# Kernel tuning notes

Hardware: AMD Instinct MI355X
Metric: run time of the kernel (lower is better)

Reference implementation:

```python
import jax, jax.numpy as jnp
import numpy as np

N = 100000
E = 1600000
IN_C, HID_C, OUT_C = 64, 64, 32


def setup_inputs() -> dict:
    key = jax.random.key(0)
    ks = jax.random.split(key, 8)
    x = jax.random.normal(ks[0], (N, IN_C), dtype=jnp.float32)
    edge_index = jax.random.randint(ks[1], (2, E), 0, N, dtype=jnp.int64)
    # GCNConv weights (glorot-ish scale) and biases
    W1 = jax.random.normal(ks[2], (IN_C, HID_C), dtype=jnp.float32) / np.sqrt(IN_C)
    b1 = jnp.zeros((HID_C,), dtype=jnp.float32)
    W2 = jax.random.normal(ks[3], (HID_C, HID_C), dtype=jnp.float32) / np.sqrt(HID_C)
    b2 = jnp.zeros((HID_C,), dtype=jnp.float32)
    Wlin = jax.random.normal(ks[4], (HID_C, OUT_C), dtype=jnp.float32) / np.sqrt(HID_C)
    blin = jnp.zeros((OUT_C,), dtype=jnp.float32)
    return {"x": x, "edge_index": edge_index, "W1": W1, "b1": b1,
            "W2": W2, "b2": b2, "Wlin": Wlin, "blin": blin}


def _gcn_norm(edge_index):
    # PyG GCNConv default: add self-loops, symmetric normalization.
    loop = jnp.arange(N, dtype=edge_index.dtype)
    row = jnp.concatenate([edge_index[0], loop])  # source nodes [E+N]
    col = jnp.concatenate([edge_index[1], loop])  # target nodes [E+N]
    deg = jax.ops.segment_sum(jnp.ones_like(col, dtype=jnp.float32), col,
                              num_segments=N)
    dinv = jnp.where(deg > 0, deg ** -0.5, 0.0)
    norm = dinv[row] * dinv[col]  # [E+N]
    return row, col, norm


def _gcn_conv(h, W, b, row, col, norm):
    h = h @ W                                  # [N, F_out]
    msg = h[row] * norm[:, None]               # gather + scale, [E+N, F_out]
    out = jax.ops.segment_sum(msg, col, num_segments=N)  # scatter-add
    return out + b


def reference(x, edge_index, W1, b1, W2, b2, Wlin, blin):
    row, col, norm = _gcn_norm(edge_index)
    h = jax.nn.relu(_gcn_conv(x, W1, b1, row, col, norm))
    h = jax.nn.relu(_gcn_conv(h, W2, b2, row, col, norm))
    return h @ Wlin + blin
```

## Files before the change

### kernel.cpp

```cpp
#include <hip/hip_runtime.h>
#include <hip/hip_fp16.h>

#define IN_C 64
#define HID_C 64
#define OUT_C 32
#define S_NODES  512
#define S_CAP  12288
#define CHUNK_E 2048

typedef _Float16 f16_t;
typedef f16_t f16x2 __attribute__((ext_vector_type(2)));

__device__ __forceinline__ float dot2(unsigned int a, unsigned int b, float c) {
#if __has_builtin(__builtin_amdgcn_fdot2)
    return __builtin_amdgcn_fdot2(*(f16x2*)&a, *(f16x2*)&b, c, false);
#else
    float2 af = __half22float2(*(__half2*)&a);
    float2 bf = __half22float2(*(__half2*)&b);
    return fmaf(af.x, bf.x, fmaf(af.y, bf.y, c));
#endif
}

__global__ void prep(const int* ei32, int* flag, int n_check,
                     const float* __restrict__ W1, const float* __restrict__ W2,
                     const float* __restrict__ Wlin,
                     unsigned short* __restrict__ Wh1,
                     unsigned short* __restrict__ Wh2,
                     unsigned short* __restrict__ Whl) {
    __shared__ int s_any;
    if (threadIdx.x == 0) s_any = 0;
    __syncthreads();
    int any = 0;
    for (int i = threadIdx.x; i < n_check; i += blockDim.x) {
        if (ei32[2 * i + 1] != 0) any = 1;
    }
    if (any) atomicOr(&s_any, 1);
    for (int i = threadIdx.x; i < 4096; i += 256) {
        int r = i >> 6, c = i & 63;
        f16_t h1 = (f16_t)W1[r * 64 + c];
        f16_t h2 = (f16_t)W2[r * 64 + c];
        Wh1[c * 64 + r] = *(unsigned short*)&h1;
        Wh2[c * 64 + r] = *(unsigned short*)&h2;
    }
    for (int i = threadIdx.x; i < 2048; i += 256) {
        int r = i >> 5, c = i & 31;
        f16_t h = (f16_t)Wlin[r * 32 + c];
        Whl[c * 64 + r] = *(unsigned short*)&h;
    }
    __syncthreads();
    if (threadIdx.x == 0) *flag = (s_any == 0) ? 1 : 0;
}

__device__ __forceinline__ int ld_edge(const void* ei, int idx, int is64) {
    if (is64) return (int)((const long long*)ei)[idx];
    return ((const int*)ei)[idx];
}

__global__ __launch_bounds__(256) void bin_edges(const void* ei, int E, const int* flag,
                                                 int* bcur, int NB,
                                                 int* __restrict__ staging) {
    __shared__ int cnt[256], boff[256], lcur[256], gbase[256];
    __shared__ int stg[CHUNK_E];
    __shared__ int s_is64;
    int tid = threadIdx.x;
    if (tid == 0) s_is64 = *flag;
    cnt[tid] = 0;
    __syncthreads();
    int is64 = s_is64;
    int e0 = blockIdx.x * CHUNK_E;
    int e1 = min(E, e0 + CHUNK_E);
    for (int e = e0 + tid; e < e1; e += 256) {
        int dst = ld_edge(ei, E + e, is64);
        atomicAdd(&cnt[dst >> 9], 1);
    }
    __syncthreads();
    int v = cnt[tid];
    gbase[tid] = v;
    __syncthreads();
    for (int o = 1; o < 256; o <<= 1) {
        int u = (tid >= o) ? gbase[tid - o] : 0;
        __syncthreads();
        gbase[tid] += u;
        __syncthreads();
    }
    boff[tid] = gbase[tid] - v;
    lcur[tid] = boff[tid];
    __syncthreads();
    for (int e = e0 + tid; e < e1; e += 256) {
        int src = ld_edge(ei, e, is64);
        int dst = ld_edge(ei, E + e, is64);
        int p = atomicAdd(&lcur[dst >> 9], 1);
        stg[p] = src | ((dst & 511) << 17);
    }
    __syncthreads();
    if (tid < NB && cnt[tid] > 0) gbase[tid] = atomicAdd(&bcur[tid], cnt[tid]);
    __syncthreads();
    int sw = tid >> 4, sl = tid & 15;
    for (int b = sw; b < NB; b += 16) {
        int c = cnt[b];
        if (c == 0) continue;
        int o = boff[b], g = gbase[b];
        size_t gb = (size_t)b * S_CAP;
        for (int j = sl; j < c; j += 16) {
            if (g + j < S_CAP) staging[gb + g + j] = stg[o + j];
        }
    }
}

__global__ __launch_bounds__(256) void place_fine(const int* __restrict__ staging,
                                                  const int* __restrict__ bcur,
                                                  int* __restrict__ offs,
                                                  float* __restrict__ dinv,
                                                  int* __restrict__ rec, int N, int NB) {
    __shared__ int sdeg[S_NODES];
    __shared__ int tsum[256];
    __shared__ int curs[S_NODES];
    __shared__ int sb[256];
    int tid = threadIdx.x;
    int vcnt = (tid < NB) ? min(bcur[tid], S_CAP) : 0;
    sb[tid] = vcnt;
    sdeg[tid] = 0;
    sdeg[tid + 256] = 0;
    __syncthreads();
    for (int o = 1; o < 256; o <<= 1) {
        int u = (tid >= o) ? sb[tid - o] : 0;
        __syncthreads();
        sb[tid] += u;
        __syncthreads();
    }
    int cnt = min(bcur[blockIdx.x], S_CAP);
    int bbase = sb[blockIdx.x] - cnt;
    if (blockIdx.x == NB - 1 && tid == 0) offs[N] = sb[255];
    int base = blockIdx.x * S_NODES;
    int nn = min(S_NODES, N - base);
    size_t sbase = (size_t)blockIdx.x * S_CAP;
    for (int j = tid; j < cnt; j += 256) atomicAdd(&sdeg[staging[sbase + j] >> 17], 1);
    __syncthreads();
    int d0 = sdeg[2 * tid], d1 = sdeg[2 * tid + 1];
    tsum[tid] = d0 + d1;
    __syncthreads();
    for (int o = 1; o < 256; o <<= 1) {
        int v = (tid >= o) ? tsum[tid - o] : 0;
        __syncthreads();
        tsum[tid] += v;
        __syncthreads();
    }
    int pre = bbase + ((tid == 0) ? 0 : tsum[tid - 1]);
    curs[2 * tid] = pre;
    curs[2 * tid + 1] = pre + d0;
    if (2 * tid < nn) {
        offs[base + 2 * tid] = pre;
        dinv[base + 2 * tid] = rsqrtf((float)(d0 + 1));
    }
    if (2 * tid + 1 < nn) {
        offs[base + 2 * tid + 1] = pre + d0;
        dinv[base + 2 * tid + 1] = rsqrtf((float)(d1 + 1));
    }
    __syncthreads();
    for (int j = tid; j < cnt; j += 256) {
        int pk = staging[sbase + j];
        int p = atomicAdd(&curs[pk >> 17], 1);
        rec[p] = pk & 0x1FFFF;
    }
}

template <int IN_F32>
__global__ __launch_bounds__(256) void gemm64(const void* __restrict__ in,
                                              const unsigned short* __restrict__ Wh,
                                              unsigned short* __restrict__ out,
                                              const float* __restrict__ dinv, int n) {
    __shared__ uint4 sA[32 * 8];
    int tid = threadIdx.x;
    int lane = tid & 63, wave = tid >> 6;
    unsigned int wu[32];
    {
        const uint4* col = (const uint4*)(Wh + (size_t)lane * 64);
#pragma unroll
        for (int j = 0; j < 8; j++) {
            uint4 w4 = col[j];
            wu[4 * j] = w4.x; wu[4 * j + 1] = w4.y;
            wu[4 * j + 2] = w4.z; wu[4 * j + 3] = w4.w;
        }
    }
    int base = blockIdx.x * 32;
    if (IN_F32) {
        const float2* A2 = (const float2*)in;
        int lim = n * 32;
        for (int i = tid; i < 1024; i += 256) {
            int gi = base * 32 + i;
            float2 v = (gi < lim) ? A2[gi] : make_float2(0.f, 0.f);
            ((__half2*)sA)[i] = __floats2half2_rn(v.x, v.y);
        }
    } else {
        const uint2* A2 = (const uint2*)in;
        int lim = n * 16;
        for (int i = tid; i < 512; i += 256) {
            int gi = base * 16 + i;
            ((uint2*)sA)[i] = (gi < lim) ? A2[gi] : make_uint2(0u, 0u);
        }
    }
    __syncthreads();
    int r0 = base + wave * 8;
    int r1 = min(r0 + 8, n);
    for (int r = r0; r < r1; r++) {
        int rr = r - base;
        float a0 = 0.f, a1 = 0.f;
#pragma unroll
        for (int j = 0; j < 8; j++) {
            uint4 u = sA[rr * 8 + j];
            a0 = dot2(u.x, wu[4 * j], a0);
            a1 = dot2(u.y, wu[4 * j + 1], a1);
            a0 = dot2(u.z, wu[4 * j + 2], a0);
            a1 = dot2(u.w, wu[4 * j + 3], a1);
        }
        __half hv = __float2half_rn((a0 + a1) * dinv[r]);
        out[(size_t)r * 64 + lane] = *(unsigned short*)&hv;
    }
}

__global__ void aggregate(const unsigned short* __restrict__ t,
                          const int* __restrict__ offs, const int* __restrict__ rec,
                          const float* __restrict__ dinv, const float* __restrict__ bias,
                          unsigned short* __restrict__ acc, int n) {
    int wave = (blockIdx.x * blockDim.x + threadIdx.x) >> 6;
    int lane = threadIdx.x & 63;
    if (wave >= n) return;
    int g = lane >> 3;
    int gl = lane & 7;
    int beg = offs[wave], end = offs[wave + 1];
    int m = end - beg + 1;
    const uint4* t4 = (const uint4*)t;
    float s[8] = {0.f, 0.f, 0.f, 0.f, 0.f, 0.f, 0.f, 0.f};
    for (int i = 0; i < m; i += 32) {
        int srcs[4];
        float ws[4];
#pragma unroll
        for (int u = 0; u < 4; u++) {
            int it = i + u * 8 + g;
            srcs[u] = (it == 0) ? wave : ((it < m) ? rec[beg + it - 1] : wave);
            ws[u] = (it < m) ? 1.f : 0.f;
        }
        uint4 vs[4];
#pragma unroll
        for (int u = 0; u < 4; u++) vs[u] = t4[(size_t)srcs[u] * 8 + gl];
#pragma unroll
        for (int u = 0; u < 4; u++) {
            float w = ws[u];
            float2 f0 = __half22float2(*(__half2*)&vs[u].x);
            float2 f1 = __half22float2(*(__half2*)&vs[u].y);
            float2 f2 = __half22float2(*(__half2*)&vs[u].z);
            float2 f3 = __half22float2(*(__half2*)&vs[u].w);
            s[0] = fmaf(f0.x, w, s[0]);
            s[1] = fmaf(f0.y, w, s[1]);
            s[2] = fmaf(f1.x, w, s[2]);
            s[3] = fmaf(f1.y, w, s[3]);
            s[4] = fmaf(f2.x, w, s[4]);
            s[5] = fmaf(f2.y, w, s[5]);
            s[6] = fmaf(f3.x, w, s[6]);
            s[7] = fmaf(f3.y, w, s[7]);
        }
    }
#pragma unroll
    for (int k = 0; k < 8; k++) {
        s[k] += __shfl_xor(s[k], 8);
        s[k] += __shfl_xor(s[k], 16);
        s[k] += __shfl_xor(s[k], 32);
    }
    if (g == 0) {
        float d = dinv[wave];
        const float4* b4 = (const float4*)bias;
        float4 bb0 = b4[gl * 2], bb1 = b4[gl * 2 + 1];
        float o0 = fmaxf(fmaf(s[0], d, bb0.x), 0.f);
        float o1 = fmaxf(fmaf(s[1], d, bb0.y), 0.f);
        float o2 = fmaxf(fmaf(s[2], d, bb0.z), 0.f);
        float o3 = fmaxf(fmaf(s[3], d, bb0.w), 0.f);
        float o4 = fmaxf(fmaf(s[4], d, bb1.x), 0.f);
        float o5 = fmaxf(fmaf(s[5], d, bb1.y), 0.f);
        float o6 = fmaxf(fmaf(s[6], d, bb1.z), 0.f);
        float o7 = fmaxf(fmaf(s[7], d, bb1.w), 0.f);
        __half2 p0 = __floats2half2_rn(o0, o1);
        __half2 p1 = __floats2half2_rn(o2, o3);
        __half2 p2 = __floats2half2_rn(o4, o5);
        __half2 p3 = __floats2half2_rn(o6, o7);
        ((uint4*)acc)[(size_t)wave * 8 + gl] =
            make_uint4(*(unsigned int*)&p0, *(unsigned int*)&p1,
                       *(unsigned int*)&p2, *(unsigned int*)&p3);
    }
}

__global__ __launch_bounds__(256) void gemm32(const unsigned short* __restrict__ in,
                                              const unsigned short* __restrict__ Wh,
                                              const float* __restrict__ b,
                                              float* __restrict__ out, int n) {
    __shared__ uint4 sA[32 * 8];
    int tid = threadIdx.x;
    int lane = tid & 63, wave = tid >> 6;
    int c = lane & 31;
    unsigned int wu[32];
    {
        const uint4* col = (const uint4*)(Wh + (size_t)c * 64);
#pragma unroll
        for (int j = 0; j < 8; j++) {
            uint4 w4 = col[j];
            wu[4 * j] = w4.x; wu[4 * j + 1] = w4.y;
            wu[4 * j + 2] = w4.z; wu[4 * j + 3] = w4.w;
        }
    }
    float bl = b[c];
    int base = blockIdx.x * 32;
    const uint2* A2 = (const uint2*)in;
    int lim = n * 16;
    for (int i = tid; i < 512; i += 256) {
        int gi = base * 16 + i;
        ((uint2*)sA)[i] = (gi < lim) ? A2[gi] : make_uint2(0u, 0u);
    }
    __syncthreads();
    int r0 = base + wave * 8;
    int r1 = min(r0 + 8, n);
    for (int r = r0; r < r1; r++) {
        int rr = r - base;
        float a0 = 0.f, a1 = 0.f;
#pragma unroll
        for (int j = 0; j < 8; j++) {
            uint4 u = sA[rr * 8 + j];
            a0 = dot2(u.x, wu[4 * j], a0);
            a1 = dot2(u.y, wu[4 * j + 1], a1);
            a0 = dot2(u.z, wu[4 * j + 2], a0);
            a1 = dot2(u.w, wu[4 * j + 3], a1);
        }
        if (lane < 32) out[(size_t)r * 32 + c] = bl + a0 + a1;
    }
}

extern "C" void kernel_launch(void* const* d_in, const int* in_sizes, int n_in,
                              void* d_out, int out_size, void* d_ws, size_t ws_size,
                              hipStream_t stream) {
    (void)n_in; (void)out_size; (void)ws_size;
    const float* x    = (const float*)d_in[0];
    const void*  ei   = d_in[1];
    const float* W1   = (const float*)d_in[2];
    const float* b1   = (const float*)d_in[3];
    const float* W2   = (const float*)d_in[4];
    const float* b2   = (const float*)d_in[5];
    const float* Wlin = (const float*)d_in[6];
    const float* blin = (const float*)d_in[7];
    float* out = (float*)d_out;

    const int N = in_sizes[0] / IN_C;
    const int E = in_sizes[1] / 2;
    const int NB = (N + S_NODES - 1) / S_NODES;
    const int NEB = (E + CHUNK_E - 1) / CHUNK_E;

    char* ws = (char*)d_ws;
    size_t off = 0;
    auto alloc = [&](size_t bytes) -> void* {
        size_t a = (off + 255) & ~(size_t)255;
        off = a + bytes;
        return (void*)(ws + a);
    };
    int*   flag    = (int*)  alloc(4);
    int*   offs    = (int*)  alloc((size_t)(N + 1) * 4);
    float* dinv    = (float*)alloc((size_t)N * 4);
    int*   bcur    = (int*)  alloc((size_t)NB * 4);
    int*   rec     = (int*)  alloc((size_t)E * 4);
    int*   staging = (int*)  alloc((size_t)NB * S_CAP * 4);
    unsigned short* tbuf = (unsigned short*)alloc((size_t)N * HID_C * 2);
    unsigned short* acc  = (unsigned short*)alloc((size_t)N * HID_C * 2);
    unsigned short* Wh1  = (unsigned short*)alloc(64 * 64 * 2);
    unsigned short* Wh2  = (unsigned short*)alloc(64 * 64 * 2);
    unsigned short* Whl  = (unsigned short*)alloc(64 * 32 * 2);

    hipMemsetAsync(bcur, 0, (size_t)NB * 4, stream);

    int n_check = E < 4096 ? E : 4096;
    prep<<<1, 256, 0, stream>>>((const int*)ei, flag, n_check, W1, W2, Wlin,
                                Wh1, Wh2, Whl);
    bin_edges<<<NEB, 256, 0, stream>>>(ei, E, flag, bcur, NB, staging);
    place_fine<<<NB, 256, 0, stream>>>(staging, bcur, offs, dinv, rec, N, NB);

    const int GB = (N + 31) / 32;
    gemm64<1><<<GB, 256, 0, stream>>>(x, Wh1, tbuf, dinv, N);
    aggregate<<<(N + 3) / 4, 256, 0, stream>>>(tbuf, offs, rec, dinv, b1, acc, N);
    gemm64<0><<<GB, 256, 0, stream>>>(acc, Wh2, tbuf, dinv, N);
    aggregate<<<(N + 3) / 4, 256, 0, stream>>>(tbuf, offs, rec, dinv, b2, acc, N);
    gemm32<<<GB, 256, 0, stream>>>(acc, Whl, blin, out, N);
}
```

Baseline: 287.5 us.

## Fuse edge binning, first GEMM and weight prep into one heterogeneous launch

Merges the prep, bin_edges and first gemm64 kernels into one launch whose blocks are split by index into edge-binning blocks, first-layer GEMM blocks and a weight-conversion block. Because the first GEMM now runs before degrees are known, the source-side dinv scaling moves into the first aggregation as a per-edge gathered weight. The int64 detection is done per block on a small sample instead of in a separate kernel. This removes two launches and lets the independent GEMM overlap the binning, at the cost of an extra dinv gather per edge in layer one and W1 being converted in every GEMM block with strided loads.

```diff
diff --git a/kernel.cpp b/kernel.cpp
--- a/kernel.cpp
+++ b/kernel.cpp
@@ -21,88 +21,121 @@
 #endif
 }
 
-__global__ void prep(const int* ei32, int* flag, int n_check,
-                     const float* __restrict__ W1, const float* __restrict__ W2,
-                     const float* __restrict__ Wlin,
-                     unsigned short* __restrict__ Wh1,
-                     unsigned short* __restrict__ Wh2,
-                     unsigned short* __restrict__ Whl) {
-    __shared__ int s_any;
-    if (threadIdx.x == 0) s_any = 0;
-    __syncthreads();
-    int any = 0;
-    for (int i = threadIdx.x; i < n_check; i += blockDim.x) {
-        if (ei32[2 * i + 1] != 0) any = 1;
-    }
-    if (any) atomicOr(&s_any, 1);
-    for (int i = threadIdx.x; i < 4096; i += 256) {
-        int r = i >> 6, c = i & 63;
-        f16_t h1 = (f16_t)W1[r * 64 + c];
-        f16_t h2 = (f16_t)W2[r * 64 + c];
-        Wh1[c * 64 + r] = *(unsigned short*)&h1;
-        Wh2[c * 64 + r] = *(unsigned short*)&h2;
-    }
-    for (int i = threadIdx.x; i < 2048; i += 256) {
-        int r = i >> 5, c = i & 31;
-        f16_t h = (f16_t)Wlin[r * 32 + c];
-        Whl[c * 64 + r] = *(unsigned short*)&h;
-    }
-    __syncthreads();
-    if (threadIdx.x == 0) *flag = (s_any == 0) ? 1 : 0;
-}
-
 __device__ __forceinline__ int ld_edge(const void* ei, int idx, int is64) {
     if (is64) return (int)((const long long*)ei)[idx];
     return ((const int*)ei)[idx];
 }
 
-__global__ __launch_bounds__(256) void bin_edges(const void* ei, int E, const int* flag,
-                                                 int* bcur, int NB,
-                                                 int* __restrict__ staging) {
-    __shared__ int cnt[256], boff[256], lcur[256], gbase[256];
-    __shared__ int stg[CHUNK_E];
-    __shared__ int s_is64;
+__global__ __launch_bounds__(256) void fat(const void* ei, int E,
+                                           int* bcur, int NB,
+                                           int* __restrict__ staging,
+                                           int NEB, int GB,
+                                           const float* __restrict__ x,
+                                           const float* __restrict__ W1,
+                                           unsigned short* __restrict__ tbuf, int n,
+                                           const float* __restrict__ W2,
+                                           const float* __restrict__ Wlin,
+                                           unsigned short* __restrict__ Wh2,
+                                           unsigned short* __restrict__ Whl) {
+    __shared__ __align__(16) int smem[3073];
     int tid = threadIdx.x;
-    if (tid == 0) s_is64 = *flag;
-    cnt[tid] = 0;
-    __syncthreads();
-    int is64 = s_is64;
-    int e0 = blockIdx.x * CHUNK_E;
-    int e1 = min(E, e0 + CHUNK_E);
-    for (int e = e0 + tid; e < e1; e += 256) {
-        int dst = ld_edge(ei, E + e, is64);
-        atomicAdd(&cnt[dst >> 9], 1);
-    }
-    __syncthreads();
-    int v = cnt[tid];
-    gbase[tid] = v;
-    __syncthreads();
-    for (int o = 1; o < 256; o <<= 1) {
-        int u = (tid >= o) ? gbase[tid - o] : 0;
-        __syncthreads();
-        gbase[tid] += u;
-        __syncthreads();
-    }
-    boff[tid] = gbase[tid] - v;
-    lcur[tid] = boff[tid];
-    __syncthreads();
-    for (int e = e0 + tid; e < e1; e += 256) {
-        int src = ld_edge(ei, e, is64);
-        int dst = ld_edge(ei, E + e, is64);
-        int p = atomicAdd(&lcur[dst >> 9], 1);
-        stg[p] = src | ((dst & 511) << 17);
-    }
-    __syncthreads();
-    if (tid < NB && cnt[tid] > 0) gbase[tid] = atomicAdd(&bcur[tid], cnt[tid]);
-    __syncthreads();
-    int sw = tid >> 4, sl = tid & 15;
-    for (int b = sw; b < NB; b += 16) {
-        int c = cnt[b];
-        if (c == 0) continue;
-        int o = boff[b], g = gbase[b];
-        size_t gb = (size_t)b * S_CAP;
-        for (int j = sl; j < c; j += 16) {
-            if (g + j < S_CAP) staging[gb + g + j] = stg[o + j];
+    int b = blockIdx.x;
+    if (b < NEB) {
+        int* cnt = smem;          int* boff = smem + 256;
+        int* lcur = smem + 512;   int* gbase = smem + 768;
+        int* stg = smem + 1024;
+        int* ps64 = smem + 3072;
+        if (tid == 0) *ps64 = 1;
+        cnt[tid] = 0;
+        __syncthreads();
+        if (2 * tid + 1 < 2 * E && ((const int*)ei)[2 * tid + 1] != 0) *ps64 = 0;
+        __syncthreads();
+        int is64 = *ps64;
+        int e0 = b * CHUNK_E;
+        int e1 = min(E, e0 + CHUNK_E);
+        for (int e = e0 + tid; e < e1; e += 256) {
+            int dst = ld_edge(ei, E + e, is64);
+            atomicAdd(&cnt[dst >> 9], 1);
+        }
+        __syncthreads();
+        int v = cnt[tid];
+        gbase[tid] = v;
+        __syncthreads();
+        for (int o = 1; o < 256; o <<= 1) {
+            int u = (tid >= o) ? gbase[tid - o] : 0;
+            __syncthreads();
+            gbase[tid] += u;
+            __syncthreads();
+        }
+        boff[tid] = gbase[tid] - v;
+        lcur[tid] = boff[tid];
+        __syncthreads();
+        for (int e = e0 + tid; e < e1; e += 256) {
+            int src = ld_edge(ei, e, is64);
+            int dst = ld_edge(ei, E + e, is64);
+            int p = atomicAdd(&lcur[dst >> 9], 1);
+            stg[p] = src | ((dst & 511) << 17);
+        }
+        __syncthreads();
+        if (tid < NB && cnt[tid] > 0) gbase[tid] = atomicAdd(&bcur[tid], cnt[tid]);
+        __syncthreads();
+        int sw = tid >> 4, sl = tid & 15;
+        for (int bk = sw; bk < NB; bk += 16) {
+            int c = cnt[bk];
+            if (c == 0) continue;
+            int o = boff[bk], g = gbase[bk];
+            size_t gb = (size_t)bk * S_CAP;
+            for (int j = sl; j < c; j += 16) {
+                if (g + j < S_CAP) staging[gb + g + j] = stg[o + j];
+            }
+        }
+    } else if (b < NEB + GB) {
+        uint4* sA = (uint4*)smem;
+        int bb = b - NEB;
+        int lane = tid & 63, wave = tid >> 6;
+        unsigned int wu[32];
+#pragma unroll
+        for (int k = 0; k < 32; k++) {
+            f16x2 p;
+            p.x = (f16_t)W1[(2 * k) * 64 + lane];
+            p.y = (f16_t)W1[(2 * k + 1) * 64 + lane];
+            wu[k] = *(unsigned int*)&p;
+        }
+        int base = bb * 32;
+        const float2* A2 = (const float2*)x;
+        int lim = n * 32;
+        for (int i = tid; i < 1024; i += 256) {
+            int gi = base * 32 + i;
+            float2 v = (gi < lim) ? A2[gi] : make_float2(0.f, 0.f);
+            ((__half2*)sA)[i] = __floats2half2_rn(v.x, v.y);
+        }
+        __syncthreads();
+        int r0 = base + wave * 8;
+        int r1 = min(r0 + 8, n);
+        for (int r = r0; r < r1; r++) {
+            int rr = r - base;
+            float a0 = 0.f, a1 = 0.f;
+#pragma unroll
+            for (int j = 0; j < 8; j++) {
+                uint4 u = sA[rr * 8 + j];
+                a0 = dot2(u.x, wu[4 * j], a0);
+                a1 = dot2(u.y, wu[4 * j + 1], a1);
+                a0 = dot2(u.z, wu[4 * j + 2], a0);
+                a1 = dot2(u.w, wu[4 * j + 3], a1);
+            }
+            __half hv = __float2half_rn(a0 + a1);
+            tbuf[(size_t)r * 64 + lane] = *(unsigned short*)&hv;
+        }
+    } else {
+        for (int i = tid; i < 4096; i += 256) {
+            int r = i >> 6, c = i & 63;
+            f16_t h2 = (f16_t)W2[r * 64 + c];
+            Wh2[c * 64 + r] = *(unsigned short*)&h2;
+        }
+        for (int i = tid; i < 2048; i += 256) {
+            int r = i >> 5, c = i & 31;
+            f16_t h = (f16_t)Wlin[r * 32 + c];
+            Whl[c * 64 + r] = *(unsigned short*)&h;
         }
     }
 }
@@ -164,60 +197,7 @@
     }
 }
 
-template <int IN_F32>
-__global__ __launch_bounds__(256) void gemm64(const void* __restrict__ in,
-                                              const unsigned short* __restrict__ Wh,
-                                              unsigned short* __restrict__ out,
-                                              const float* __restrict__ dinv, int n) {
-    __shared__ uint4 sA[32 * 8];
-    int tid = threadIdx.x;
-    int lane = tid & 63, wave = tid >> 6;
-    unsigned int wu[32];
-    {
-        const uint4* col = (const uint4*)(Wh + (size_t)lane * 64);
-#pragma unroll
-        for (int j = 0; j < 8; j++) {
-            uint4 w4 = col[j];
-            wu[4 * j] = w4.x; wu[4 * j + 1] = w4.y;
-            wu[4 * j + 2] = w4.z; wu[4 * j + 3] = w4.w;
-        }
-    }
-    int base = blockIdx.x * 32;
-    if (IN_F32) {
-        const float2* A2 = (const float2*)in;
-        int lim = n * 32;
-        for (int i = tid; i < 1024; i += 256) {
-            int gi = base * 32 + i;
-            float2 v = (gi < lim) ? A2[gi] : make_float2(0.f, 0.f);
-            ((__half2*)sA)[i] = __floats2half2_rn(v.x, v.y);
-        }
-    } else {
-        const uint2* A2 = (const uint2*)in;
-        int lim = n * 16;
-        for (int i = tid; i < 512; i += 256) {
-            int gi = base * 16 + i;
-            ((uint2*)sA)[i] = (gi < lim) ? A2[gi] : make_uint2(0u, 0u);
-        }
-    }
-    __syncthreads();
-    int r0 = base + wave * 8;
-    int r1 = min(r0 + 8, n);
-    for (int r = r0; r < r1; r++) {
-        int rr = r - base;
-        float a0 = 0.f, a1 = 0.f;
-#pragma unroll
-        for (int j = 0; j < 8; j++) {
-            uint4 u = sA[rr * 8 + j];
-            a0 = dot2(u.x, wu[4 * j], a0);
-            a1 = dot2(u.y, wu[4 * j + 1], a1);
-            a0 = dot2(u.z, wu[4 * j + 2], a0);
-            a1 = dot2(u.w, wu[4 * j + 3], a1);
-        }
-        __half hv = __float2half_rn((a0 + a1) * dinv[r]);
-        out[(size_t)r * 64 + lane] = *(unsigned short*)&hv;
-    }
-}
-
+template <int WDINV>
 __global__ void aggregate(const unsigned short* __restrict__ t,
                           const int* __restrict__ offs, const int* __restrict__ rec,
                           const float* __restrict__ dinv, const float* __restrict__ bias,
@@ -238,7 +218,12 @@
         for (int u = 0; u < 4; u++) {
             int it = i + u * 8 + g;
             srcs[u] = (it == 0) ? wave : ((it < m) ? rec[beg + it - 1] : wave);
-            ws[u] = (it < m) ? 1.f : 0.f;
+            if (WDINV) {
+                float dv = dinv[srcs[u]];
+                ws[u] = (it < m) ? dv : 0.f;
+            } else {
+                ws[u] = (it < m) ? 1.f : 0.f;
+            }
         }
         uint4 vs[4];
 #pragma unroll
@@ -288,6 +273,49 @@
     }
 }
 
+__global__ __launch_bounds__(256) void gemm64(const unsigned short* __restrict__ in,
+                                              const unsigned short* __restrict__ Wh,
+                                              unsigned short* __restrict__ out,
+                                              const float* __restrict__ dinv, int n) {
+    __shared__ uint4 sA[32 * 8];
+    int tid = threadIdx.x;
+    int lane = tid & 63, wave = tid >> 6;
+    unsigned int wu[32];
+    {
+        const uint4* col = (const uint4*)(Wh + (size_t)lane * 64);
+#pragma unroll
+        for (int j = 0; j < 8; j++) {
+            uint4 w4 = col[j];
+            wu[4 * j] = w4.x; wu[4 * j + 1] = w4.y;
+            wu[4 * j + 2] = w4.z; wu[4 * j + 3] = w4.w;
+        }
+    }
+    int base = blockIdx.x * 32;
+    const uint2* A2 = (const uint2*)in;
+    int lim = n * 16;
+    for (int i = tid; i < 512; i += 256) {
+        int gi = base * 16 + i;
+        ((uint2*)sA)[i] = (gi < lim) ? A2[gi] : make_uint2(0u, 0u);
+    }
+    __syncthreads();
+    int r0 = base + wave * 8;
+    int r1 = min(r0 + 8, n);
+    for (int r = r0; r < r1; r++) {
+        int rr = r - base;
+        float a0 = 0.f, a1 = 0.f;
+#pragma unroll
+        for (int j = 0; j < 8; j++) {
+            uint4 u = sA[rr * 8 + j];
+            a0 = dot2(u.x, wu[4 * j], a0);
+            a1 = dot2(u.y, wu[4 * j + 1], a1);
+            a0 = dot2(u.z, wu[4 * j + 2], a0);
+            a1 = dot2(u.w, wu[4 * j + 3], a1);
+        }
+        __half hv = __float2half_rn((a0 + a1) * dinv[r]);
+        out[(size_t)r * 64 + lane] = *(unsigned short*)&hv;
+    }
+}
+
 __global__ __launch_bounds__(256) void gemm32(const unsigned short* __restrict__ in,
                                               const unsigned short* __restrict__ Wh,
                                               const float* __restrict__ b,
@@ -350,6 +378,7 @@
     const int E = in_sizes[1] / 2;
     const int NB = (N + S_NODES - 1) / S_NODES;
     const int NEB = (E + CHUNK_E - 1) / CHUNK_E;
+    const int GB = (N + 31) / 32;
 
     char* ws = (char*)d_ws;
     size_t off = 0;
@@ -358,7 +387,6 @@
         off = a + bytes;
         return (void*)(ws + a);
     };
-    int*   flag    = (int*)  alloc(4);
     int*   offs    = (int*)  alloc((size_t)(N + 1) * 4);
     float* dinv    = (float*)alloc((size_t)N * 4);
     int*   bcur    = (int*)  alloc((size_t)NB * 4);
@@ -366,22 +394,17 @@
     int*   staging = (int*)  alloc((size_t)NB * S_CAP * 4);
     unsigned short* tbuf = (unsigned short*)alloc((size_t)N * HID_C * 2);
     unsigned short* acc  = (unsigned short*)alloc((size_t)N * HID_C * 2);
-    unsigned short* Wh1  = (unsigned short*)alloc(64 * 64 * 2);
     unsigned short* Wh2  = (unsigned short*)alloc(64 * 64 * 2);
     unsigned short* Whl  = (unsigned short*)alloc(64 * 32 * 2);
 
     hipMemsetAsync(bcur, 0, (size_t)NB * 4, stream);
 
-    int n_check = E < 4096 ? E : 4096;
-    prep<<<1, 256, 0, stream>>>((const int*)ei, flag, n_check, W1, W2, Wlin,
-                                Wh1, Wh2, Whl);
-    bin_edges<<<NEB, 256, 0, stream>>>(ei, E, flag, bcur, NB, staging);
+    fat<<<NEB + GB + 1, 256, 0, stream>>>(ei, E, bcur, NB, staging, NEB, GB,
+                                          x, W1, tbuf, N, W2, Wlin, Wh2, Whl);
     place_fine<<<NB, 256, 0, stream>>>(staging, bcur, offs, dinv, rec, N, NB);
 
-    const int GB = (N + 31) / 32;
-    gemm64<1><<<GB, 256, 0, stream>>>(x, Wh1, tbuf, dinv, N);
-    aggregate<<<(N + 3) / 4, 256, 0, stream>>>(tbuf, offs, rec, dinv, b1, acc, N);
-    gemm64<0><<<GB, 256, 0, stream>>>(acc, Wh2, tbuf, dinv, N);
-    aggregate<<<(N + 3) / 4, 256, 0, stream>>>(tbuf, offs, rec, dinv, b2, acc, N);
+    aggregate<1><<<(N + 3) / 4, 256, 0, stream>>>(tbuf, offs, rec, dinv, b1, acc, N);
+    gemm64<<<GB, 256, 0, stream>>>(acc, Wh2, tbuf, dinv, N);
+    aggregate<0><<<(N + 3) / 4, 256, 0, stream>>>(tbuf, offs, rec, dinv, b2, acc, N);
     gemm32<<<GB, 256, 0, stream>>>(acc, Whl, blin, out, N);
 }
```

After: 266.5 us. -7.3%, faster.
